# Kernel tuning notes

Measured on AMD Instinct MI355X. Metric: run time of the kernel, lower is better.

The kernel has to match this reference:

```python
import jax, jax.numpy as jnp
import numpy as np

N_NODES = 50000
N_EDGES = 800000
D_IN, D_HID, D_OUT, D_EDGE = 128, 256, 128, 16


def setup_inputs() -> dict:
    key = jax.random.key(0)
    ks = jax.random.split(key, 6)
    nh = jax.random.normal(ks[0], (N_NODES, D_IN), dtype=jnp.float32)
    eh = jax.random.normal(ks[1], (N_EDGES, D_EDGE), dtype=jnp.float32)
    edge_index = jax.random.randint(ks[2], (2, N_EDGES), 0, N_NODES, dtype=jnp.int32)
    # MLP params (build_layer: Linear(d_in,d_hid) -> relu -> Linear(d_hid,d_out)), scaled init
    W1 = jax.random.normal(ks[3], (D_IN, D_HID), dtype=jnp.float32) / np.sqrt(D_IN)
    b1 = jnp.zeros((D_HID,), dtype=jnp.float32)
    W2 = jax.random.normal(ks[4], (D_HID, D_OUT), dtype=jnp.float32) / np.sqrt(D_HID)
    b2 = jnp.zeros((D_OUT,), dtype=jnp.float32)
    return {"nh": nh, "eh": eh, "edge_index": edge_index,
            "W1": W1, "b1": b1, "W2": W2, "b2": b2}


def reference(nh, eh, edge_index, W1, b1, W2, b2):
    n_nodes = nh.shape[0]
    # nf_lin: 2-layer MLP with relu
    n_h = jax.nn.relu(nh @ W1 + b1) @ W2 + b2          # [N, d]
    src, dst = edge_index[0], edge_index[1]
    src_nh = n_h[src]                                   # [E, d] gather
    dst_nh = n_h[dst]                                   # [E, d] gather
    attn = jnp.sum(src_nh * dst_nh, axis=-1)            # [E] per-edge score
    # segment softmax over edges grouped by destination node
    seg_max = jax.ops.segment_max(attn, dst, num_segments=n_nodes)  # [N]
    e = jnp.exp(attn - seg_max[dst])                    # [E] stable exp
    denom = jax.ops.segment_sum(e, dst, num_segments=n_nodes)       # [N]
    attn = e / denom[dst]                               # [E]
    # weighted scatter-add aggregation
    nz = jax.ops.segment_sum(attn[:, None] * src_nh, dst, num_segments=n_nodes)  # [N, d]
    return (n_h + nz, eh)
```

## Files before the change

### kernel.cpp

```cpp
#include <hip/hip_runtime.h>
#include <math.h>


#define D_IN   128
#define D_HID  256
#define D_OUT  128

typedef short bf16x8 __attribute__((ext_vector_type(8)));
typedef float f32x4  __attribute__((ext_vector_type(4)));

__device__ __forceinline__ short f2bf(float f)
{
    unsigned int u = __float_as_uint(f);
    unsigned int r = (u + 0x7fffu + ((u >> 16) & 1u)) >> 16;
    return (short)r;
}
__device__ __forceinline__ float bf2f(short h)
{
    return __uint_as_float(((unsigned int)(unsigned short)h) << 16);
}

__device__ __forceinline__ void pack_body(const float* __restrict__ W,
                                          short* __restrict__ Bh,
                                          short* __restrict__ Bl,
                                          int K, int N, int u)
{
    const int T = K >> 5;
    const int l = u & 63;
    const int t = (u >> 6) % T;
    const int c = u / (64 * T);
    const int lr = l & 15, kb = l >> 4;
    bf16x8 vh, vl;
#pragma unroll
    for (int j = 0; j < 8; ++j) {
        int k   = t * 32 + kb * 8 + j;
        int col = c * 16 + lr;
        float x = W[(size_t)k * N + col];
        short hi = f2bf(x);
        vh[j] = hi;
        vl[j] = f2bf(x - bf2f(hi));
    }
    *(bf16x8*)(Bh + (size_t)u * 8) = vh;
    *(bf16x8*)(Bl + (size_t)u * 8) = vl;
}

#define PREP_COPY_BLOCKS 1024

__global__ __launch_bounds__(256)
void prep(const float* __restrict__ eh, float* __restrict__ out_eh, int n4,
          const float* __restrict__ A, short* __restrict__ Ah,
          short* __restrict__ Al, long valid, long total8, int nAB,
          const float* __restrict__ W1, short* __restrict__ B1h,
          short* __restrict__ B1l,
          const float* __restrict__ W2, short* __restrict__ B2h,
          short* __restrict__ B2l)
{
    int b = blockIdx.x;
    const int tid = threadIdx.x;
    if (b < PREP_COPY_BLOCKS) {
        const float4* in4 = (const float4*)eh;
        float4* o4 = (float4*)out_eh;
        for (int i = b * 256 + tid; i < n4; i += PREP_COPY_BLOCKS * 256)
            o4[i] = in4[i];
        return;
    }
    b -= PREP_COPY_BLOCKS;
    if (b < nAB) {
        long t = (long)b * 256 + tid;
        if (t < total8) {
            long base = t * 8;
            bf16x8 vh, vl;
            if (base < valid) {
                float4 f0 = *(const float4*)(A + base);
                float4 f1 = *(const float4*)(A + base + 4);
                float fv[8] = {f0.x, f0.y, f0.z, f0.w, f1.x, f1.y, f1.z, f1.w};
#pragma unroll
                for (int j = 0; j < 8; ++j) {
                    short hi = f2bf(fv[j]);
                    vh[j] = hi;
                    vl[j] = f2bf(fv[j] - bf2f(hi));
                }
            } else {
                vh = (bf16x8)0; vl = (bf16x8)0;
            }
            *(bf16x8*)(Ah + base) = vh;
            *(bf16x8*)(Al + base) = vl;
        }
        return;
    }
    b -= nAB;
    if (b < 16) pack_body(W1, B1h, B1l, D_IN, D_HID, b * 256 + tid);
    else        pack_body(W2, B2h, B2l, D_HID, D_OUT, (b - 16) * 256 + tid);
}

#define H_STRIDE 136

__global__ __launch_bounds__(256)
void mlp_fused(const short* __restrict__ Ah, const short* __restrict__ Al,
               const short* __restrict__ B1h, const short* __restrict__ B1l,
               const float* __restrict__ b1,
               const short* __restrict__ B2h, const short* __restrict__ B2l,
               const float* __restrict__ b2,
               float* __restrict__ out, short* __restrict__ nhb, int Nvalid)
{
    __shared__ __attribute__((aligned(16))) short Hh[64 * H_STRIDE];
    __shared__ __attribute__((aligned(16))) short Hl[64 * H_STRIDE];

    const int w  = threadIdx.x >> 6;
    const int l  = threadIdx.x & 63;
    const int lr = l & 15, kb = l >> 4;
    const size_t row0 = (size_t)blockIdx.x * 64;

    f32x4 acc2[4][2] = {};

#pragma unroll
    for (int h = 0; h < 2; ++h) {
        f32x4 acc1[4][2] = {};
#pragma unroll
        for (int t = 0; t < 4; ++t) {
            bf16x8 ah[4], al[4], bh[2], bl[2];
#pragma unroll
            for (int m = 0; m < 4; ++m) {
                size_t aoff = (row0 + m * 16 + lr) * D_IN + t * 32 + kb * 8;
                ah[m] = *(const bf16x8*)(Ah + aoff);
                al[m] = *(const bf16x8*)(Al + aoff);
            }
#pragma unroll
            for (int n = 0; n < 2; ++n) {
                int c = h * 8 + w * 2 + n;
                size_t boff = (size_t)((c * 4 + t) * 64 + l) * 8;
                bh[n] = *(const bf16x8*)(B1h + boff);
                bl[n] = *(const bf16x8*)(B1l + boff);
            }
#pragma unroll
            for (int m = 0; m < 4; ++m)
#pragma unroll
                for (int n = 0; n < 2; ++n) {
                    acc1[m][n] = __builtin_amdgcn_mfma_f32_16x16x32_bf16(ah[m], bh[n], acc1[m][n], 0, 0, 0);
                    acc1[m][n] = __builtin_amdgcn_mfma_f32_16x16x32_bf16(al[m], bh[n], acc1[m][n], 0, 0, 0);
                    acc1[m][n] = __builtin_amdgcn_mfma_f32_16x16x32_bf16(ah[m], bl[n], acc1[m][n], 0, 0, 0);
                }
        }
        if (h) __syncthreads();
#pragma unroll
        for (int n = 0; n < 2; ++n) {
            int lcol = w * 32 + n * 16 + lr;
            float bb = b1[h * 128 + lcol];
#pragma unroll
            for (int m = 0; m < 4; ++m)
#pragma unroll
                for (int i = 0; i < 4; ++i) {
                    int lrow = m * 16 + kb * 4 + i;
                    float v = fmaxf(acc1[m][n][i] + bb, 0.f);
                    short hi = f2bf(v);
                    Hh[lrow * H_STRIDE + lcol] = hi;
                    Hl[lrow * H_STRIDE + lcol] = f2bf(v - bf2f(hi));
                }
        }
        __syncthreads();

#pragma unroll
        for (int t2 = 0; t2 < 4; ++t2) {
            bf16x8 ah[4], al[4], bh[2], bl[2];
#pragma unroll
            for (int m = 0; m < 4; ++m) {
                const int lo = (m * 16 + lr) * H_STRIDE + t2 * 32 + kb * 8;
                ah[m] = *(const bf16x8*)&Hh[lo];
                al[m] = *(const bf16x8*)&Hl[lo];
            }
#pragma unroll
            for (int n = 0; n < 2; ++n) {
                int c = w * 2 + n;
                size_t boff = (size_t)((c * 8 + (h * 4 + t2)) * 64 + l) * 8;
                bh[n] = *(const bf16x8*)(B2h + boff);
                bl[n] = *(const bf16x8*)(B2l + boff);
            }
#pragma unroll
            for (int m = 0; m < 4; ++m)
#pragma unroll
                for (int n = 0; n < 2; ++n) {
                    acc2[m][n] = __builtin_amdgcn_mfma_f32_16x16x32_bf16(ah[m], bh[n], acc2[m][n], 0, 0, 0);
                    acc2[m][n] = __builtin_amdgcn_mfma_f32_16x16x32_bf16(al[m], bh[n], acc2[m][n], 0, 0, 0);
                    acc2[m][n] = __builtin_amdgcn_mfma_f32_16x16x32_bf16(ah[m], bl[n], acc2[m][n], 0, 0, 0);
                }
        }
    }

#pragma unroll
    for (int n = 0; n < 2; ++n) {
        int col = w * 32 + n * 16 + lr;
        float bb = b2[col];
#pragma unroll
        for (int m = 0; m < 4; ++m)
#pragma unroll
            for (int i = 0; i < 4; ++i) {
                size_t row = row0 + m * 16 + kb * 4 + i;
                float v = acc2[m][n][i] + bb;
                nhb[row * D_OUT + col] = f2bf(v);
                if ((int)row < Nvalid) out[row * D_OUT + col] = v;
            }
    }
}

__global__ __launch_bounds__(256)
void hist_pos(const int* __restrict__ dst, unsigned int* __restrict__ count,
              unsigned int* __restrict__ pos, int E)
{
    int e = blockIdx.x * blockDim.x + threadIdx.x;
    if (e < E) pos[e] = atomicAdd(count + dst[e], 1u);
}

__global__ __launch_bounds__(256)
void chunk_sums(const unsigned int* __restrict__ count,
                unsigned int* __restrict__ bsum, int n)
{
    __shared__ unsigned int lds[256];
    const int t = threadIdx.x;
    const int i = blockIdx.x * 256 + t;
    lds[t] = (i < n) ? count[i] : 0u;
    __syncthreads();
#pragma unroll
    for (int d = 128; d > 0; d >>= 1) {
        if (t < d) lds[t] += lds[t + d];
        __syncthreads();
    }
    if (t == 0) bsum[blockIdx.x] = lds[0];
}

__global__ __launch_bounds__(256)
void scan_sums(const unsigned int* __restrict__ bsum,
               unsigned int* __restrict__ boff, int nb)
{
    __shared__ unsigned int lds[256];
    const int t = threadIdx.x;
    unsigned int v = (t < nb) ? bsum[t] : 0u;
    lds[t] = v;
    __syncthreads();
#pragma unroll
    for (int d = 1; d < 256; d <<= 1) {
        unsigned int x = lds[t];
        unsigned int add = (t >= d) ? lds[t - d] : 0u;
        __syncthreads();
        lds[t] = x + add;
        __syncthreads();
    }
    if (t < nb) boff[t] = lds[t] - v;
}

__global__ __launch_bounds__(256)
void write_off(const unsigned int* __restrict__ count,
               const unsigned int* __restrict__ boff,
               unsigned int* __restrict__ off, int n)
{
    __shared__ unsigned int lds[256];
    const int t = threadIdx.x;
    const int i = blockIdx.x * 256 + t;
    unsigned int v = (i < n) ? count[i] : 0u;
    lds[t] = v;
    __syncthreads();
#pragma unroll
    for (int d = 1; d < 256; d <<= 1) {
        unsigned int x = lds[t];
        unsigned int add = (t >= d) ? lds[t - d] : 0u;
        __syncthreads();
        lds[t] = x + add;
        __syncthreads();
    }
    unsigned int incl = lds[t];
    unsigned int base = boff[blockIdx.x];
    if (i < n)  off[i] = base + incl - v;
    if (i == n - 1) off[n] = base + incl;
}

__global__ __launch_bounds__(256)
void fill_srcs(const int* __restrict__ src, const int* __restrict__ dst,
               const unsigned int* __restrict__ off,
               const unsigned int* __restrict__ pos,
               int* __restrict__ srcs, int E)
{
    int e = blockIdx.x * blockDim.x + threadIdx.x;
    if (e >= E) return;
    srcs[off[dst[e]] + pos[e]] = src[e];
}

#define NEG_HUGE -3.0e38f

__global__ __launch_bounds__(256)
void node_aggregate(const short* __restrict__ nhb,
                    const unsigned int* __restrict__ off,
                    const int* __restrict__ srcs,
                    float* __restrict__ out, int N)
{
    int wid  = (blockIdx.x * blockDim.x + threadIdx.x) >> 6;
    int lane = threadIdx.x & 63;
    if (wid >= N) return;
    const int g = lane >> 4;
    const int j = lane & 15;

    const float* sp = out + (size_t)wid * D_OUT + j * 8;
    const float4 sa = *(const float4*)sp;
    const float4 sb = *(const float4*)(sp + 4);

    const unsigned int beg = off[wid];
    const unsigned int end = off[wid + 1];

    float m = NEG_HUGE, den = 0.f;
    float c0 = 0.f, c1 = 0.f, c2 = 0.f, c3 = 0.f;
    float c4 = 0.f, c5 = 0.f, c6 = 0.f, c7 = 0.f;

    for (unsigned int base = beg; base < end; base += 4) {
        unsigned int idx = base + g;
        bool valid = idx < end;
        int sidx = valid ? srcs[idx] : 0;
        uint4 av = *(const uint4*)(nhb + (size_t)sidx * D_OUT + j * 8);
        float a0 = __uint_as_float(av.x << 16);
        float a1 = __uint_as_float(av.x & 0xffff0000u);
        float a2 = __uint_as_float(av.y << 16);
        float a3 = __uint_as_float(av.y & 0xffff0000u);
        float a4 = __uint_as_float(av.z << 16);
        float a5 = __uint_as_float(av.z & 0xffff0000u);
        float a6 = __uint_as_float(av.w << 16);
        float a7 = __uint_as_float(av.w & 0xffff0000u);

        float p = a0 * sa.x + a1 * sa.y + a2 * sa.z + a3 * sa.w
                + a4 * sb.x + a5 * sb.y + a6 * sb.z + a7 * sb.w;
        p += __shfl_xor(p, 1);
        p += __shfl_xor(p, 2);
        p += __shfl_xor(p, 4);
        p += __shfl_xor(p, 8);

        float pv    = valid ? p : NEG_HUGE;
        float mnew  = fmaxf(m, pv);
        float scale = __expf(m - mnew);
        float wgt   = valid ? __expf(p - mnew) : 0.f;
        den = fmaf(den, scale, wgt);
        c0 = fmaf(c0, scale, wgt * a0);
        c1 = fmaf(c1, scale, wgt * a1);
        c2 = fmaf(c2, scale, wgt * a2);
        c3 = fmaf(c3, scale, wgt * a3);
        c4 = fmaf(c4, scale, wgt * a4);
        c5 = fmaf(c5, scale, wgt * a5);
        c6 = fmaf(c6, scale, wgt * a6);
        c7 = fmaf(c7, scale, wgt * a7);
        m = mnew;
    }

#pragma unroll
    for (int o = 16; o < 64; o <<= 1) {
        float m2 = __shfl_xor(m, o);
        float d2 = __shfl_xor(den, o);
        float b0 = __shfl_xor(c0, o), b1 = __shfl_xor(c1, o);
        float b2v = __shfl_xor(c2, o), b3 = __shfl_xor(c3, o);
        float b4 = __shfl_xor(c4, o), b5 = __shfl_xor(c5, o);
        float b6 = __shfl_xor(c6, o), b7 = __shfl_xor(c7, o);
        float mn = fmaxf(m, m2);
        float s1 = __expf(m - mn);
        float s2 = __expf(m2 - mn);
        den = den * s1 + d2 * s2;
        c0 = c0 * s1 + b0 * s2;  c1 = c1 * s1 + b1 * s2;
        c2 = c2 * s1 + b2v * s2; c3 = c3 * s1 + b3 * s2;
        c4 = c4 * s1 + b4 * s2;  c5 = c5 * s1 + b5 * s2;
        c6 = c6 * s1 + b6 * s2;  c7 = c7 * s1 + b7 * s2;
        m = mn;
    }

    float inv = (den > 0.f) ? 1.f / den : 0.f;
    if (g == 0) {
        float4 o0, o1;
        o0.x = sa.x + c0 * inv; o0.y = sa.y + c1 * inv;
        o0.z = sa.z + c2 * inv; o0.w = sa.w + c3 * inv;
        o1.x = sb.x + c4 * inv; o1.y = sb.y + c5 * inv;
        o1.z = sb.z + c6 * inv; o1.w = sb.w + c7 * inv;
        float* op = out + (size_t)wid * D_OUT + j * 8;
        *(float4*)op = o0;
        *(float4*)(op + 4) = o1;
    }
}

extern "C" void kernel_launch(void* const* d_in, const int* in_sizes, int n_in,
                              void* d_out, int out_size, void* d_ws, size_t ws_size,
                              hipStream_t stream)
{
    const float* nh  = (const float*)d_in[0];
    const float* eh  = (const float*)d_in[1];
    const int*   ei  = (const int*)d_in[2];
    const float* W1  = (const float*)d_in[3];
    const float* b1  = (const float*)d_in[4];
    const float* W2  = (const float*)d_in[5];
    const float* b2  = (const float*)d_in[6];

    const int N  = in_sizes[0] / D_IN;
    const int E  = in_sizes[2] / 2;
    const int EH = in_sizes[1];
    const int Mp = (N + 63) & ~63;
    const int NB = (N + 255) / 256;

    const int* src = ei;
    const int* dst = ei + E;

    float* out_nh = (float*)d_out;
    float* out_eh = (float*)d_out + (size_t)N * D_OUT;

    char* ws = (char*)d_ws;
    size_t o = 0;
    short* Ahp = (short*)(ws + o); o += (size_t)Mp * D_IN * 2;
    short* Alp = (short*)(ws + o); o += (size_t)Mp * D_IN * 2;
    short* nhb = (short*)(ws + o); o += (size_t)Mp * D_OUT * 2;
    short* B1h = (short*)(ws + o); o += (size_t)D_IN  * D_HID * 2;
    short* B1l = (short*)(ws + o); o += (size_t)D_IN  * D_HID * 2;
    short* B2h = (short*)(ws + o); o += (size_t)D_HID * D_OUT * 2;
    short* B2l = (short*)(ws + o); o += (size_t)D_HID * D_OUT * 2;
    int*          srcs  = (int*)(ws + o);          o += (size_t)E * 4;
    unsigned int* pos   = (unsigned int*)(ws + o); o += (size_t)E * 4;
    unsigned int* count = (unsigned int*)(ws + o); o += (size_t)N * 4;
    unsigned int* off   = (unsigned int*)(ws + o); o += (size_t)(N + 1) * 4;
    unsigned int* bsum  = (unsigned int*)(ws + o); o += (size_t)NB * 4;
    unsigned int* boff  = (unsigned int*)(ws + o); o += (size_t)NB * 4;

    {
        long total8 = (long)Mp * D_IN / 8;
        int  nAB    = (int)((total8 + 255) / 256);
        prep<<<PREP_COPY_BLOCKS + nAB + 32, 256, 0, stream>>>(
            eh, out_eh, EH / 4,
            nh, Ahp, Alp, (long)N * D_IN, total8, nAB,
            W1, B1h, B1l, W2, B2h, B2l);
    }

    hipMemsetAsync(count, 0, (size_t)N * 4, stream);
    hist_pos<<<(E + 255) / 256, 256, 0, stream>>>(dst, count, pos, E);
    chunk_sums<<<NB, 256, 0, stream>>>(count, bsum, N);
    scan_sums<<<1, 256, 0, stream>>>(bsum, boff, NB);
    write_off<<<NB, 256, 0, stream>>>(count, boff, off, N);
    fill_srcs<<<(E + 255) / 256, 256, 0, stream>>>(src, dst, off, pos, srcs, E);

    mlp_fused<<<Mp / 64, 256, 0, stream>>>(Ahp, Alp, B1h, B1l, b1,
                                           B2h, B2l, b2, out_nh, nhb, N);

    node_aggregate<<<(N + 3) / 4, 256, 0, stream>>>(nhb, off, srcs, out_nh, N);
}
```

Baseline: 175.1 us.

## Fuse histogram into prep kernel and drop low-part of hidden activations

The per-edge destination histogram (atomic count plus position) now runs as extra blocks of the prep kernel, which removes one kernel launch and lets it overlap with the copy and packing work. Separately, the second MLP GEMM no longer keeps the low bf16 residual of the hidden activations. That removes one LDS buffer, its stores and loads, and one of the three MFMAs per tile. The precision cut lowers accuracy of the hidden layer to plain bf16, which risks tolerance failures.

```diff
diff --git a/kernel.cpp b/kernel.cpp
--- a/kernel.cpp
+++ b/kernel.cpp
@@ -53,7 +53,9 @@
           const float* __restrict__ W1, short* __restrict__ B1h,
           short* __restrict__ B1l,
           const float* __restrict__ W2, short* __restrict__ B2h,
-          short* __restrict__ B2l)
+          short* __restrict__ B2l,
+          const int* __restrict__ dst, unsigned int* __restrict__ count,
+          unsigned int* __restrict__ pos, int E)
 {
     int b = blockIdx.x;
     const int tid = threadIdx.x;
@@ -89,8 +91,14 @@
         return;
     }
     b -= nAB;
-    if (b < 16) pack_body(W1, B1h, B1l, D_IN, D_HID, b * 256 + tid);
-    else        pack_body(W2, B2h, B2l, D_HID, D_OUT, (b - 16) * 256 + tid);
+    if (b < 32) {
+        if (b < 16) pack_body(W1, B1h, B1l, D_IN, D_HID, b * 256 + tid);
+        else        pack_body(W2, B2h, B2l, D_HID, D_OUT, (b - 16) * 256 + tid);
+        return;
+    }
+    b -= 32;
+    int e = b * 256 + tid;
+    if (e < E) pos[e] = atomicAdd(count + dst[e], 1u);
 }
 
 #define H_STRIDE 136
@@ -104,7 +112,6 @@
                float* __restrict__ out, short* __restrict__ nhb, int Nvalid)
 {
     __shared__ __attribute__((aligned(16))) short Hh[64 * H_STRIDE];
-    __shared__ __attribute__((aligned(16))) short Hl[64 * H_STRIDE];
 
     const int w  = threadIdx.x >> 6;
     const int l  = threadIdx.x & 63;
@@ -152,22 +159,17 @@
                 for (int i = 0; i < 4; ++i) {
                     int lrow = m * 16 + kb * 4 + i;
                     float v = fmaxf(acc1[m][n][i] + bb, 0.f);
-                    short hi = f2bf(v);
-                    Hh[lrow * H_STRIDE + lcol] = hi;
-                    Hl[lrow * H_STRIDE + lcol] = f2bf(v - bf2f(hi));
+                    Hh[lrow * H_STRIDE + lcol] = f2bf(v);
                 }
         }
         __syncthreads();
 
 #pragma unroll
         for (int t2 = 0; t2 < 4; ++t2) {
-            bf16x8 ah[4], al[4], bh[2], bl[2];
-#pragma unroll
-            for (int m = 0; m < 4; ++m) {
-                const int lo = (m * 16 + lr) * H_STRIDE + t2 * 32 + kb * 8;
-                ah[m] = *(const bf16x8*)&Hh[lo];
-                al[m] = *(const bf16x8*)&Hl[lo];
-            }
+            bf16x8 ah[4], bh[2], bl[2];
+#pragma unroll
+            for (int m = 0; m < 4; ++m)
+                ah[m] = *(const bf16x8*)&Hh[(m * 16 + lr) * H_STRIDE + t2 * 32 + kb * 8];
 #pragma unroll
             for (int n = 0; n < 2; ++n) {
                 int c = w * 2 + n;
@@ -180,7 +182,6 @@
 #pragma unroll
                 for (int n = 0; n < 2; ++n) {
                     acc2[m][n] = __builtin_amdgcn_mfma_f32_16x16x32_bf16(ah[m], bh[n], acc2[m][n], 0, 0, 0);
-                    acc2[m][n] = __builtin_amdgcn_mfma_f32_16x16x32_bf16(al[m], bh[n], acc2[m][n], 0, 0, 0);
                     acc2[m][n] = __builtin_amdgcn_mfma_f32_16x16x32_bf16(ah[m], bl[n], acc2[m][n], 0, 0, 0);
                 }
         }
@@ -200,14 +201,6 @@
                 if ((int)row < Nvalid) out[row * D_OUT + col] = v;
             }
     }
-}
-
-__global__ __launch_bounds__(256)
-void hist_pos(const int* __restrict__ dst, unsigned int* __restrict__ count,
-              unsigned int* __restrict__ pos, int E)
-{
-    int e = blockIdx.x * blockDim.x + threadIdx.x;
-    if (e < E) pos[e] = atomicAdd(count + dst[e], 1u);
 }
 
 __global__ __launch_bounds__(256)
@@ -417,17 +410,18 @@
     unsigned int* bsum  = (unsigned int*)(ws + o); o += (size_t)NB * 4;
     unsigned int* boff  = (unsigned int*)(ws + o); o += (size_t)NB * 4;
 
+    hipMemsetAsync(count, 0, (size_t)N * 4, stream);
     {
         long total8 = (long)Mp * D_IN / 8;
         int  nAB    = (int)((total8 + 255) / 256);
-        prep<<<PREP_COPY_BLOCKS + nAB + 32, 256, 0, stream>>>(
+        int  histB  = (E + 255) / 256;
+        prep<<<PREP_COPY_BLOCKS + nAB + 32 + histB, 256, 0, stream>>>(
             eh, out_eh, EH / 4,
             nh, Ahp, Alp, (long)N * D_IN, total8, nAB,
-            W1, B1h, B1l, W2, B2h, B2l);
-    }
-
-    hipMemsetAsync(count, 0, (size_t)N * 4, stream);
-    hist_pos<<<(E + 255) / 256, 256, 0, stream>>>(dst, count, pos, E);
+            W1, B1h, B1l, W2, B2h, B2l,
+            dst, count, pos, E);
+    }
+
     chunk_sums<<<NB, 256, 0, stream>>>(count, bsum, N);
     scan_sums<<<1, 256, 0, stream>>>(bsum, boff, NB);
     write_off<<<NB, 256, 0, stream>>>(count, boff, off, N);
```

Result: slower. 184.4 us (+5.3%).

## Merge MLP with edge fill kernel, halve MLP tile rows, drop hidden low-part

Applied to the files above, without the earlier changes.

Folds the fill_srcs scatter into the MLP kernel as extra blocks, so both run in one launch and can overlap. The MLP tile shrinks from 64 to 32 rows per block, which doubles the block count and reduces registers and LDS per block. The hidden activation is now stored only as a single bf16 value with no low residual, which removes one LDS array and one MFMA per step in the second GEMM. This lowers the precision of the second layer, and the workspace padding changes to a multiple of 32 rows.

```diff
diff --git a/kernel.cpp b/kernel.cpp
--- a/kernel.cpp
+++ b/kernel.cpp
@@ -93,34 +93,52 @@
     else        pack_body(W2, B2h, B2l, D_HID, D_OUT, (b - 16) * 256 + tid);
 }
 
+__global__ __launch_bounds__(256)
+void hist_pos(const int* __restrict__ dst, unsigned int* __restrict__ count,
+              unsigned int* __restrict__ pos, int E)
+{
+    int e = blockIdx.x * blockDim.x + threadIdx.x;
+    if (e < E) pos[e] = atomicAdd(count + dst[e], 1u);
+}
+
 #define H_STRIDE 136
 
 __global__ __launch_bounds__(256)
-void mlp_fused(const short* __restrict__ Ah, const short* __restrict__ Al,
-               const short* __restrict__ B1h, const short* __restrict__ B1l,
-               const float* __restrict__ b1,
-               const short* __restrict__ B2h, const short* __restrict__ B2l,
-               const float* __restrict__ b2,
-               float* __restrict__ out, short* __restrict__ nhb, int Nvalid)
-{
-    __shared__ __attribute__((aligned(16))) short Hh[64 * H_STRIDE];
-    __shared__ __attribute__((aligned(16))) short Hl[64 * H_STRIDE];
+void mlp_and_fill(const short* __restrict__ Ah, const short* __restrict__ Al,
+                  const short* __restrict__ B1h, const short* __restrict__ B1l,
+                  const float* __restrict__ b1,
+                  const short* __restrict__ B2h, const short* __restrict__ B2l,
+                  const float* __restrict__ b2,
+                  float* __restrict__ out, short* __restrict__ nhb, int Nvalid,
+                  int mlpB,
+                  const int* __restrict__ src, const int* __restrict__ dst,
+                  const unsigned int* __restrict__ off,
+                  const unsigned int* __restrict__ pos,
+                  int* __restrict__ srcs, int E)
+{
+    __shared__ __attribute__((aligned(16))) short Hh[32 * H_STRIDE];
+
+    if (blockIdx.x >= mlpB) {
+        int e = (blockIdx.x - mlpB) * 256 + threadIdx.x;
+        if (e < E) srcs[off[dst[e]] + pos[e]] = src[e];
+        return;
+    }
 
     const int w  = threadIdx.x >> 6;
     const int l  = threadIdx.x & 63;
     const int lr = l & 15, kb = l >> 4;
-    const size_t row0 = (size_t)blockIdx.x * 64;
-
-    f32x4 acc2[4][2] = {};
+    const size_t row0 = (size_t)blockIdx.x * 32;
+
+    f32x4 acc2[2][2] = {};
 
 #pragma unroll
     for (int h = 0; h < 2; ++h) {
-        f32x4 acc1[4][2] = {};
+        f32x4 acc1[2][2] = {};
 #pragma unroll
         for (int t = 0; t < 4; ++t) {
-            bf16x8 ah[4], al[4], bh[2], bl[2];
-#pragma unroll
-            for (int m = 0; m < 4; ++m) {
+            bf16x8 ah[2], al[2], bh[2], bl[2];
+#pragma unroll
+            for (int m = 0; m < 2; ++m) {
                 size_t aoff = (row0 + m * 16 + lr) * D_IN + t * 32 + kb * 8;
                 ah[m] = *(const bf16x8*)(Ah + aoff);
                 al[m] = *(const bf16x8*)(Al + aoff);
@@ -133,7 +151,7 @@
                 bl[n] = *(const bf16x8*)(B1l + boff);
             }
 #pragma unroll
-            for (int m = 0; m < 4; ++m)
+            for (int m = 0; m < 2; ++m)
 #pragma unroll
                 for (int n = 0; n < 2; ++n) {
                     acc1[m][n] = __builtin_amdgcn_mfma_f32_16x16x32_bf16(ah[m], bh[n], acc1[m][n], 0, 0, 0);
@@ -147,27 +165,22 @@
             int lcol = w * 32 + n * 16 + lr;
             float bb = b1[h * 128 + lcol];
 #pragma unroll
-            for (int m = 0; m < 4; ++m)
+            for (int m = 0; m < 2; ++m)
 #pragma unroll
                 for (int i = 0; i < 4; ++i) {
                     int lrow = m * 16 + kb * 4 + i;
                     float v = fmaxf(acc1[m][n][i] + bb, 0.f);
-                    short hi = f2bf(v);
-                    Hh[lrow * H_STRIDE + lcol] = hi;
-                    Hl[lrow * H_STRIDE + lcol] = f2bf(v - bf2f(hi));
+                    Hh[lrow * H_STRIDE + lcol] = f2bf(v);
                 }
         }
         __syncthreads();
 
 #pragma unroll
         for (int t2 = 0; t2 < 4; ++t2) {
-            bf16x8 ah[4], al[4], bh[2], bl[2];
-#pragma unroll
-            for (int m = 0; m < 4; ++m) {
-                const int lo = (m * 16 + lr) * H_STRIDE + t2 * 32 + kb * 8;
-                ah[m] = *(const bf16x8*)&Hh[lo];
-                al[m] = *(const bf16x8*)&Hl[lo];
-            }
+            bf16x8 ah[2], bh[2], bl[2];
+#pragma unroll
+            for (int m = 0; m < 2; ++m)
+                ah[m] = *(const bf16x8*)&Hh[(m * 16 + lr) * H_STRIDE + t2 * 32 + kb * 8];
 #pragma unroll
             for (int n = 0; n < 2; ++n) {
                 int c = w * 2 + n;
@@ -176,11 +189,10 @@
                 bl[n] = *(const bf16x8*)(B2l + boff);
             }
 #pragma unroll
-            for (int m = 0; m < 4; ++m)
+            for (int m = 0; m < 2; ++m)
 #pragma unroll
                 for (int n = 0; n < 2; ++n) {
                     acc2[m][n] = __builtin_amdgcn_mfma_f32_16x16x32_bf16(ah[m], bh[n], acc2[m][n], 0, 0, 0);
-                    acc2[m][n] = __builtin_amdgcn_mfma_f32_16x16x32_bf16(al[m], bh[n], acc2[m][n], 0, 0, 0);
                     acc2[m][n] = __builtin_amdgcn_mfma_f32_16x16x32_bf16(ah[m], bl[n], acc2[m][n], 0, 0, 0);
                 }
         }
@@ -191,7 +203,7 @@
         int col = w * 32 + n * 16 + lr;
         float bb = b2[col];
 #pragma unroll
-        for (int m = 0; m < 4; ++m)
+        for (int m = 0; m < 2; ++m)
 #pragma unroll
             for (int i = 0; i < 4; ++i) {
                 size_t row = row0 + m * 16 + kb * 4 + i;
@@ -203,14 +215,6 @@
 }
 
 __global__ __launch_bounds__(256)
-void hist_pos(const int* __restrict__ dst, unsigned int* __restrict__ count,
-              unsigned int* __restrict__ pos, int E)
-{
-    int e = blockIdx.x * blockDim.x + threadIdx.x;
-    if (e < E) pos[e] = atomicAdd(count + dst[e], 1u);
-}
-
-__global__ __launch_bounds__(256)
 void chunk_sums(const unsigned int* __restrict__ count,
                 unsigned int* __restrict__ bsum, int n)
 {
@@ -270,17 +274,6 @@
     unsigned int base = boff[blockIdx.x];
     if (i < n)  off[i] = base + incl - v;
     if (i == n - 1) off[n] = base + incl;
-}
-
-__global__ __launch_bounds__(256)
-void fill_srcs(const int* __restrict__ src, const int* __restrict__ dst,
-               const unsigned int* __restrict__ off,
-               const unsigned int* __restrict__ pos,
-               int* __restrict__ srcs, int E)
-{
-    int e = blockIdx.x * blockDim.x + threadIdx.x;
-    if (e >= E) return;
-    srcs[off[dst[e]] + pos[e]] = src[e];
 }
 
 #define NEG_HUGE -3.0e38f
@@ -392,7 +385,7 @@
     const int N  = in_sizes[0] / D_IN;
     const int E  = in_sizes[2] / 2;
     const int EH = in_sizes[1];
-    const int Mp = (N + 63) & ~63;
+    const int Mp = (N + 31) & ~31;
     const int NB = (N + 255) / 256;
 
     const int* src = ei;
@@ -417,6 +410,7 @@
     unsigned int* bsum  = (unsigned int*)(ws + o); o += (size_t)NB * 4;
     unsigned int* boff  = (unsigned int*)(ws + o); o += (size_t)NB * 4;
 
+    hipMemsetAsync(count, 0, (size_t)N * 4, stream);
     {
         long total8 = (long)Mp * D_IN / 8;
         int  nAB    = (int)((total8 + 255) / 256);
@@ -426,15 +420,19 @@
             W1, B1h, B1l, W2, B2h, B2l);
     }
 
-    hipMemsetAsync(count, 0, (size_t)N * 4, stream);
     hist_pos<<<(E + 255) / 256, 256, 0, stream>>>(dst, count, pos, E);
     chunk_sums<<<NB, 256, 0, stream>>>(count, bsum, N);
     scan_sums<<<1, 256, 0, stream>>>(bsum, boff, NB);
     write_off<<<NB, 256, 0, stream>>>(count, boff, off, N);
-    fill_srcs<<<(E + 255) / 256, 256, 0, stream>>>(src, dst, off, pos, srcs, E);
-
-    mlp_fused<<<Mp / 64, 256, 0, stream>>>(Ahp, Alp, B1h, B1l, b1,
-                                           B2h, B2l, b2, out_nh, nhb, N);
+
+    {
+        int mlpB  = Mp / 32;
+        int fillB = (E + 255) / 256;
+        mlp_and_fill<<<mlpB + fillB, 256, 0, stream>>>(
+            Ahp, Alp, B1h, B1l, b1, B2h, B2l, b2,
+            out_nh, nhb, N, mlpB,
+            src, dst, off, pos, srcs, E);
+    }
 
     node_aggregate<<<(N + 3) / 4, 256, 0, stream>>>(nhb, off, srcs, out_nh, N);
 }
```

Result: faster. 168.2 us (-4.0%).

## Compute full hidden layer in one pass with single-bf16 H and move eh copy

Applied to the files above, without the earlier changes.

The MLP kernel now computes all 256 hidden columns per block in one pass (each wave covers 64 columns) instead of two halves. It stores the ReLU hidden activations in shared memory as a single bf16 value instead of a hi/lo pair, which cuts the second GEMM from three MFMAs to two per tile and halves shared-memory traffic. The edge-feature passthrough copy moves from the prep kernel into the aggregation kernel as extra blocks, so it can overlap with the gather-bound aggregation. Dropping the low half of H lowers precision of the second layer, and the larger accumulator tile raises register pressure.

```diff
diff --git a/kernel.cpp b/kernel.cpp
--- a/kernel.cpp
+++ b/kernel.cpp
@@ -44,11 +44,8 @@
     *(bf16x8*)(Bl + (size_t)u * 8) = vl;
 }
 
-#define PREP_COPY_BLOCKS 1024
-
-__global__ __launch_bounds__(256)
-void prep(const float* __restrict__ eh, float* __restrict__ out_eh, int n4,
-          const float* __restrict__ A, short* __restrict__ Ah,
+__global__ __launch_bounds__(256)
+void prep(const float* __restrict__ A, short* __restrict__ Ah,
           short* __restrict__ Al, long valid, long total8, int nAB,
           const float* __restrict__ W1, short* __restrict__ B1h,
           short* __restrict__ B1l,
@@ -57,14 +54,6 @@
 {
     int b = blockIdx.x;
     const int tid = threadIdx.x;
-    if (b < PREP_COPY_BLOCKS) {
-        const float4* in4 = (const float4*)eh;
-        float4* o4 = (float4*)out_eh;
-        for (int i = b * 256 + tid; i < n4; i += PREP_COPY_BLOCKS * 256)
-            o4[i] = in4[i];
-        return;
-    }
-    b -= PREP_COPY_BLOCKS;
     if (b < nAB) {
         long t = (long)b * 256 + tid;
         if (t < total8) {
@@ -93,7 +82,15 @@
     else        pack_body(W2, B2h, B2l, D_HID, D_OUT, (b - 16) * 256 + tid);
 }
 
-#define H_STRIDE 136
+__global__ __launch_bounds__(256)
+void hist_pos(const int* __restrict__ dst, unsigned int* __restrict__ count,
+              unsigned int* __restrict__ pos, int E)
+{
+    int e = blockIdx.x * blockDim.x + threadIdx.x;
+    if (e < E) pos[e] = atomicAdd(count + dst[e], 1u);
+}
+
+#define H2_STRIDE 264
 
 __global__ __launch_bounds__(256)
 void mlp_fused(const short* __restrict__ Ah, const short* __restrict__ Al,
@@ -103,87 +100,76 @@
                const float* __restrict__ b2,
                float* __restrict__ out, short* __restrict__ nhb, int Nvalid)
 {
-    __shared__ __attribute__((aligned(16))) short Hh[64 * H_STRIDE];
-    __shared__ __attribute__((aligned(16))) short Hl[64 * H_STRIDE];
+    __shared__ __attribute__((aligned(16))) short H[64 * H2_STRIDE];
 
     const int w  = threadIdx.x >> 6;
     const int l  = threadIdx.x & 63;
     const int lr = l & 15, kb = l >> 4;
     const size_t row0 = (size_t)blockIdx.x * 64;
 
+    f32x4 acc1[4][4] = {};
+#pragma unroll
+    for (int t = 0; t < 4; ++t) {
+        bf16x8 ah[4], al[4], bh[4], bl[4];
+#pragma unroll
+        for (int m = 0; m < 4; ++m) {
+            size_t aoff = (row0 + m * 16 + lr) * D_IN + t * 32 + kb * 8;
+            ah[m] = *(const bf16x8*)(Ah + aoff);
+            al[m] = *(const bf16x8*)(Al + aoff);
+        }
+#pragma unroll
+        for (int n = 0; n < 4; ++n) {
+            int c = w * 4 + n;
+            size_t boff = (size_t)((c * 4 + t) * 64 + l) * 8;
+            bh[n] = *(const bf16x8*)(B1h + boff);
+            bl[n] = *(const bf16x8*)(B1l + boff);
+        }
+#pragma unroll
+        for (int m = 0; m < 4; ++m)
+#pragma unroll
+            for (int n = 0; n < 4; ++n) {
+                acc1[m][n] = __builtin_amdgcn_mfma_f32_16x16x32_bf16(ah[m], bh[n], acc1[m][n], 0, 0, 0);
+                acc1[m][n] = __builtin_amdgcn_mfma_f32_16x16x32_bf16(al[m], bh[n], acc1[m][n], 0, 0, 0);
+                acc1[m][n] = __builtin_amdgcn_mfma_f32_16x16x32_bf16(ah[m], bl[n], acc1[m][n], 0, 0, 0);
+            }
+    }
+
+#pragma unroll
+    for (int n = 0; n < 4; ++n) {
+        int col = w * 64 + n * 16 + lr;
+        float bb = b1[col];
+#pragma unroll
+        for (int m = 0; m < 4; ++m)
+#pragma unroll
+            for (int i = 0; i < 4; ++i) {
+                int lrow = m * 16 + kb * 4 + i;
+                float v = fmaxf(acc1[m][n][i] + bb, 0.f);
+                H[lrow * H2_STRIDE + col] = f2bf(v);
+            }
+    }
+    __syncthreads();
+
     f32x4 acc2[4][2] = {};
-
-#pragma unroll
-    for (int h = 0; h < 2; ++h) {
-        f32x4 acc1[4][2] = {};
-#pragma unroll
-        for (int t = 0; t < 4; ++t) {
-            bf16x8 ah[4], al[4], bh[2], bl[2];
-#pragma unroll
-            for (int m = 0; m < 4; ++m) {
-                size_t aoff = (row0 + m * 16 + lr) * D_IN + t * 32 + kb * 8;
-                ah[m] = *(const bf16x8*)(Ah + aoff);
-                al[m] = *(const bf16x8*)(Al + aoff);
+#pragma unroll
+    for (int t2 = 0; t2 < 8; ++t2) {
+        bf16x8 a[4], bh[2], bl[2];
+#pragma unroll
+        for (int m = 0; m < 4; ++m)
+            a[m] = *(const bf16x8*)&H[(m * 16 + lr) * H2_STRIDE + t2 * 32 + kb * 8];
+#pragma unroll
+        for (int n = 0; n < 2; ++n) {
+            int c = w * 2 + n;
+            size_t boff = (size_t)((c * 8 + t2) * 64 + l) * 8;
+            bh[n] = *(const bf16x8*)(B2h + boff);
+            bl[n] = *(const bf16x8*)(B2l + boff);
+        }
+#pragma unroll
+        for (int m = 0; m < 4; ++m)
+#pragma unroll
+            for (int n = 0; n < 2; ++n) {
+                acc2[m][n] = __builtin_amdgcn_mfma_f32_16x16x32_bf16(a[m], bh[n], acc2[m][n], 0, 0, 0);
+                acc2[m][n] = __builtin_amdgcn_mfma_f32_16x16x32_bf16(a[m], bl[n], acc2[m][n], 0, 0, 0);
             }
-#pragma unroll
-            for (int n = 0; n < 2; ++n) {
-                int c = h * 8 + w * 2 + n;
-                size_t boff = (size_t)((c * 4 + t) * 64 + l) * 8;
-                bh[n] = *(const bf16x8*)(B1h + boff);
-                bl[n] = *(const bf16x8*)(B1l + boff);
-            }
-#pragma unroll
-            for (int m = 0; m < 4; ++m)
-#pragma unroll
-                for (int n = 0; n < 2; ++n) {
-                    acc1[m][n] = __builtin_amdgcn_mfma_f32_16x16x32_bf16(ah[m], bh[n], acc1[m][n], 0, 0, 0);
-                    acc1[m][n] = __builtin_amdgcn_mfma_f32_16x16x32_bf16(al[m], bh[n], acc1[m][n], 0, 0, 0);
-                    acc1[m][n] = __builtin_amdgcn_mfma_f32_16x16x32_bf16(ah[m], bl[n], acc1[m][n], 0, 0, 0);
-                }
-        }
-        if (h) __syncthreads();
-#pragma unroll
-        for (int n = 0; n < 2; ++n) {
-            int lcol = w * 32 + n * 16 + lr;
-            float bb = b1[h * 128 + lcol];
-#pragma unroll
-            for (int m = 0; m < 4; ++m)
-#pragma unroll
-                for (int i = 0; i < 4; ++i) {
-                    int lrow = m * 16 + kb * 4 + i;
-                    float v = fmaxf(acc1[m][n][i] + bb, 0.f);
-                    short hi = f2bf(v);
-                    Hh[lrow * H_STRIDE + lcol] = hi;
-                    Hl[lrow * H_STRIDE + lcol] = f2bf(v - bf2f(hi));
-                }
-        }
-        __syncthreads();
-
-#pragma unroll
-        for (int t2 = 0; t2 < 4; ++t2) {
-            bf16x8 ah[4], al[4], bh[2], bl[2];
-#pragma unroll
-            for (int m = 0; m < 4; ++m) {
-                const int lo = (m * 16 + lr) * H_STRIDE + t2 * 32 + kb * 8;
-                ah[m] = *(const bf16x8*)&Hh[lo];
-                al[m] = *(const bf16x8*)&Hl[lo];
-            }
-#pragma unroll
-            for (int n = 0; n < 2; ++n) {
-                int c = w * 2 + n;
-                size_t boff = (size_t)((c * 8 + (h * 4 + t2)) * 64 + l) * 8;
-                bh[n] = *(const bf16x8*)(B2h + boff);
-                bl[n] = *(const bf16x8*)(B2l + boff);
-            }
-#pragma unroll
-            for (int m = 0; m < 4; ++m)
-#pragma unroll
-                for (int n = 0; n < 2; ++n) {
-                    acc2[m][n] = __builtin_amdgcn_mfma_f32_16x16x32_bf16(ah[m], bh[n], acc2[m][n], 0, 0, 0);
-                    acc2[m][n] = __builtin_amdgcn_mfma_f32_16x16x32_bf16(al[m], bh[n], acc2[m][n], 0, 0, 0);
-                    acc2[m][n] = __builtin_amdgcn_mfma_f32_16x16x32_bf16(ah[m], bl[n], acc2[m][n], 0, 0, 0);
-                }
-        }
     }
 
 #pragma unroll
@@ -203,14 +189,6 @@
 }
 
 __global__ __launch_bounds__(256)
-void hist_pos(const int* __restrict__ dst, unsigned int* __restrict__ count,
-              unsigned int* __restrict__ pos, int E)
-{
-    int e = blockIdx.x * blockDim.x + threadIdx.x;
-    if (e < E) pos[e] = atomicAdd(count + dst[e], 1u);
-}
-
-__global__ __launch_bounds__(256)
 void chunk_sums(const unsigned int* __restrict__ count,
                 unsigned int* __restrict__ bsum, int n)
 {
@@ -286,12 +264,19 @@
 #define NEG_HUGE -3.0e38f
 
 __global__ __launch_bounds__(256)
-void node_aggregate(const short* __restrict__ nhb,
-                    const unsigned int* __restrict__ off,
-                    const int* __restrict__ srcs,
-                    float* __restrict__ out, int N)
-{
-    int wid  = (blockIdx.x * blockDim.x + threadIdx.x) >> 6;
+void agg_copy(const short* __restrict__ nhb,
+              const unsigned int* __restrict__ off,
+              const int* __restrict__ srcs,
+              float* __restrict__ out, int N,
+              const float4* __restrict__ ehin, float4* __restrict__ ehout,
+              int n4, int copyB)
+{
+    if ((int)blockIdx.x < copyB) {
+        for (int i = blockIdx.x * 256 + threadIdx.x; i < n4; i += copyB * 256)
+            ehout[i] = ehin[i];
+        return;
+    }
+    int wid  = (((int)blockIdx.x - copyB) * 256 + (int)threadIdx.x) >> 6;
     int lane = threadIdx.x & 63;
     if (wid >= N) return;
     const int g = lane >> 4;
@@ -417,16 +402,15 @@
     unsigned int* bsum  = (unsigned int*)(ws + o); o += (size_t)NB * 4;
     unsigned int* boff  = (unsigned int*)(ws + o); o += (size_t)NB * 4;
 
+    hipMemsetAsync(count, 0, (size_t)N * 4, stream);
     {
         long total8 = (long)Mp * D_IN / 8;
         int  nAB    = (int)((total8 + 255) / 256);
-        prep<<<PREP_COPY_BLOCKS + nAB + 32, 256, 0, stream>>>(
-            eh, out_eh, EH / 4,
+        prep<<<nAB + 32, 256, 0, stream>>>(
             nh, Ahp, Alp, (long)N * D_IN, total8, nAB,
             W1, B1h, B1l, W2, B2h, B2l);
     }
 
-    hipMemsetAsync(count, 0, (size_t)N * 4, stream);
     hist_pos<<<(E + 255) / 256, 256, 0, stream>>>(dst, count, pos, E);
     chunk_sums<<<NB, 256, 0, stream>>>(count, bsum, N);
     scan_sums<<<1, 256, 0, stream>>>(bsum, boff, NB);
@@ -436,5 +420,11 @@
     mlp_fused<<<Mp / 64, 256, 0, stream>>>(Ahp, Alp, B1h, B1l, b1,
                                            B2h, B2l, b2, out_nh, nhb, N);
 
-    node_aggregate<<<(N + 3) / 4, 256, 0, stream>>>(nhb, off, srcs, out_nh, N);
-}
+    {
+        int copyB = 512;
+        int aggB  = (N + 3) / 4;
+        agg_copy<<<copyB + aggB, 256, 0, stream>>>(
+            nhb, off, srcs, out_nh, N,
+            (const float4*)eh, (float4*)out_eh, EH / 4, copyB);
+    }
+}
```

Result: faster. 163.4 us (-6.7%).
